# Optimization experiments

Measured on AMD Instinct MI355X. Metric: run time of the kernel, lower is better.

The kernel has to match this reference:

```python
import jax, jax.numpy as jnp
import numpy as np

B, N, D, V = 4096, 200, 128, 100000

def setup_inputs() -> dict:
    key = jax.random.key(0)
    k1, k2, k3, k4 = jax.random.split(key, 4)
    x = jax.random.normal(k1, (B, D), dtype=jnp.float32)
    candidates = jax.random.randint(k2, (B, N), 0, V, dtype=jnp.int64)
    W_mu = jax.random.normal(k3, (D, D), dtype=jnp.float32) * (1.0 / np.sqrt(D))
    b_mu = jnp.zeros((D,), dtype=jnp.float32)
    mu_bias = jnp.zeros((V,), dtype=jnp.float32)
    emb_table = jax.random.normal(k4, (V, D), dtype=jnp.float32) * 0.02
    return {"x": x, "candidates": candidates, "W_mu": W_mu, "b_mu": b_mu,
            "mu_bias": mu_bias, "emb_table": emb_table}

def reference(x, candidates, W_mu, b_mu, mu_bias, emb_table):
    # mu_head: Linear(d_model, d_model) followed by exact (erf) GELU
    h = jax.nn.gelu(x @ W_mu + b_mu, approximate=False)          # (B, D)
    emb = emb_table[candidates]                                  # (B, N, D) gather
    logits = jnp.einsum('bd,bnd->bn', h, emb)                    # batched dot product
    logits = logits + mu_bias[candidates]                        # bias gather-add
    return logits
```

## Files before the change

kernel.cpp:

```cpp
#include <hip/hip_runtime.h>
#include <hip/hip_bf16.h>
#include <math.h>


#define BDIM 4096
#define NCAND 200
#define DDIM 128

__global__ __launch_bounds__(256) void gelu_head_kernel(
    const float* __restrict__ x, const float* __restrict__ W,
    const float* __restrict__ bvec, float* __restrict__ h) {
  __shared__ float xs[8][DDIM];
  const int b0 = blockIdx.x * 8;
  const int t = threadIdx.x;

  {
    const float4* xg = reinterpret_cast<const float4*>(x + (size_t)b0 * DDIM);
    float4* xsv = reinterpret_cast<float4*>(&xs[0][0]);
    xsv[t] = xg[t];
  }
  __syncthreads();

  const int col = t & 127;
  const int rp = t >> 7;
  float acc0 = 0.f, acc1 = 0.f, acc2 = 0.f, acc3 = 0.f;
#pragma unroll 8
  for (int k = 0; k < DDIM; ++k) {
    const float w = W[k * DDIM + col];
    acc0 = fmaf(xs[rp + 0][k], w, acc0);
    acc1 = fmaf(xs[rp + 2][k], w, acc1);
    acc2 = fmaf(xs[rp + 4][k], w, acc2);
    acc3 = fmaf(xs[rp + 6][k], w, acc3);
  }
  const float bb = bvec[col];
  float v[4] = {acc0 + bb, acc1 + bb, acc2 + bb, acc3 + bb};
#pragma unroll
  for (int r = 0; r < 4; ++r) {
    const float u = v[r];
    const float g = 0.5f * u * (1.0f + erff(u * 0.70710678118654752f));
    h[(size_t)(b0 + rp + 2 * r) * DDIM + col] = g;
  }
}

__global__ __launch_bounds__(256) void gather_dot_kernel(
    const float* __restrict__ h, const int* __restrict__ cand,
    const float* __restrict__ bias, const float* __restrict__ emb,
    float* __restrict__ out) {
  const int wave = (blockIdx.x * 256 + threadIdx.x) >> 6;
  const int lane = threadIdx.x & 63;
  const int b = wave >> 1;
  const int half = wave & 1;
  const int l16 = lane & 15;
  const int grp = lane >> 4;

  const float4* hv = reinterpret_cast<const float4*>(h + (size_t)b * DDIM);
  const float4 h1 = hv[l16];
  const float4 h2 = hv[l16 + 16];

  const int nstart = half * 100;
  const int nend = nstart + 100;
  const int rowbase = b * NCAND;

  for (int n0 = nstart; n0 < nend; n0 += 64) {
    const int nseg = min(64, nend - n0);
    int ci = 0;
    float bi = 0.f;
    if (lane < nseg) {
      ci = cand[rowbase + n0 + lane];
      bi = bias[ci];
    }
    const int iters = nseg >> 2;
#pragma unroll 4
    for (int i = 0; i < iters; ++i) {
      const int slot = i * 4 + grp;
      const int c = __shfl(ci, slot);
      const float4* ev = reinterpret_cast<const float4*>(emb + (size_t)c * DDIM);
      const float4 v1 = ev[l16];
      const float4 v2 = ev[l16 + 16];
      float acc = v1.x * h1.x;
      acc = fmaf(v1.y, h1.y, acc);
      acc = fmaf(v1.z, h1.z, acc);
      acc = fmaf(v1.w, h1.w, acc);
      acc = fmaf(v2.x, h2.x, acc);
      acc = fmaf(v2.y, h2.y, acc);
      acc = fmaf(v2.z, h2.z, acc);
      acc = fmaf(v2.w, h2.w, acc);
      acc += __shfl_xor(acc, 1);
      acc += __shfl_xor(acc, 2);
      acc += __shfl_xor(acc, 4);
      acc += __shfl_xor(acc, 8);
      const float bslot = __shfl(bi, slot);
      if (l16 == 0) out[rowbase + n0 + slot] = acc + bslot;
    }
  }
}

extern "C" void kernel_launch(void* const* d_in, const int* in_sizes, int n_in,
                              void* d_out, int out_size, void* d_ws, size_t ws_size,
                              hipStream_t stream) {
  const float* x = (const float*)d_in[0];
  const int* candidates = (const int*)d_in[1];
  const float* W_mu = (const float*)d_in[2];
  const float* b_mu = (const float*)d_in[3];
  const float* mu_bias = (const float*)d_in[4];
  const float* emb_table = (const float*)d_in[5];
  float* out = (float*)d_out;

  float* h = (float*)d_ws;

  gelu_head_kernel<<<BDIM / 8, 256, 0, stream>>>(x, W_mu, b_mu, h);
  gather_dot_kernel<<<(BDIM * 2) / 4, 256, 0, stream>>>(h, candidates, mu_bias,
                                                        emb_table, out);
}
```

Baseline: 157.5 us.

## Invert candidate gather into per-vocab CSR grouping via histogram, scan, scatter

```diff
diff --git a/kernel.cpp b/kernel.cpp
--- a/kernel.cpp
+++ b/kernel.cpp
@@ -6,6 +6,11 @@
 #define BDIM 4096
 #define NCAND 200
 #define DDIM 128
+#define VOCAB 100000
+#define NPAIRS (BDIM * NCAND)
+#define NSB ((VOCAB + 1023) / 1024)
+
+typedef unsigned int u32;
 
 __global__ __launch_bounds__(256) void gelu_head_kernel(
     const float* __restrict__ x, const float* __restrict__ W,
@@ -13,14 +18,12 @@
   __shared__ float xs[8][DDIM];
   const int b0 = blockIdx.x * 8;
   const int t = threadIdx.x;
-
   {
     const float4* xg = reinterpret_cast<const float4*>(x + (size_t)b0 * DDIM);
     float4* xsv = reinterpret_cast<float4*>(&xs[0][0]);
     xsv[t] = xg[t];
   }
   __syncthreads();
-
   const int col = t & 127;
   const int rp = t >> 7;
   float acc0 = 0.f, acc1 = 0.f, acc2 = 0.f, acc3 = 0.f;
@@ -42,6 +45,121 @@
   }
 }
 
+__global__ __launch_bounds__(256) void hist_kernel(const int* __restrict__ cand,
+                                                   u32* __restrict__ counts) {
+  const int i = blockIdx.x * 256 + threadIdx.x;
+  if (i < NPAIRS) atomicAdd(&counts[cand[i]], 1u);
+}
+
+__global__ __launch_bounds__(256) void scan1_kernel(const u32* __restrict__ counts,
+                                                    u32* __restrict__ offsets,
+                                                    u32* __restrict__ partials) {
+  __shared__ u32 sh[256];
+  const int tid = threadIdx.x;
+  const int base = blockIdx.x * 1024 + tid * 4;
+  u32 v0 = (base + 0 < VOCAB) ? counts[base + 0] : 0u;
+  u32 v1 = (base + 1 < VOCAB) ? counts[base + 1] : 0u;
+  u32 v2 = (base + 2 < VOCAB) ? counts[base + 2] : 0u;
+  u32 v3 = (base + 3 < VOCAB) ? counts[base + 3] : 0u;
+  const u32 s = v0 + v1 + v2 + v3;
+  sh[tid] = s;
+  __syncthreads();
+  for (int off = 1; off < 256; off <<= 1) {
+    const u32 t = (tid >= off) ? sh[tid - off] : 0u;
+    __syncthreads();
+    sh[tid] += t;
+    __syncthreads();
+  }
+  u32 excl = sh[tid] - s;
+  if (tid == 255) partials[blockIdx.x] = sh[255];
+  if (base + 0 < VOCAB) offsets[base + 0] = excl;
+  excl += v0;
+  if (base + 1 < VOCAB) offsets[base + 1] = excl;
+  excl += v1;
+  if (base + 2 < VOCAB) offsets[base + 2] = excl;
+  excl += v2;
+  if (base + 3 < VOCAB) offsets[base + 3] = excl;
+}
+
+__global__ __launch_bounds__(256) void scan2_kernel(u32* __restrict__ partials) {
+  __shared__ u32 sh[256];
+  const int tid = threadIdx.x;
+  const u32 p = (tid < NSB) ? partials[tid] : 0u;
+  sh[tid] = p;
+  __syncthreads();
+  for (int off = 1; off < 256; off <<= 1) {
+    const u32 t = (tid >= off) ? sh[tid - off] : 0u;
+    __syncthreads();
+    sh[tid] += t;
+    __syncthreads();
+  }
+  if (tid < NSB) partials[tid] = sh[tid] - p;
+}
+
+__global__ __launch_bounds__(256) void scan_add_kernel(u32* __restrict__ offsets,
+                                                       const u32* __restrict__ partials,
+                                                       u32* __restrict__ cursors) {
+  const int i = blockIdx.x * 256 + threadIdx.x;
+  if (i < VOCAB) {
+    const u32 v = offsets[i] + partials[i >> 10];
+    offsets[i] = v;
+    cursors[i] = v;
+  }
+  if (i == VOCAB) offsets[VOCAB] = (u32)NPAIRS;
+}
+
+__global__ __launch_bounds__(256) void scatter_kernel(const int* __restrict__ cand,
+                                                      u32* __restrict__ cursors,
+                                                      u32* __restrict__ pairs) {
+  const int i = blockIdx.x * 256 + threadIdx.x;
+  if (i < NPAIRS) {
+    const u32 c = (u32)cand[i];
+    const u32 pos = atomicAdd(&cursors[c], 1u);
+    pairs[pos] = (u32)i;
+  }
+}
+
+__global__ __launch_bounds__(256) void vocab_dot_kernel(
+    const float* __restrict__ h, const float* __restrict__ emb,
+    const float* __restrict__ bias, const u32* __restrict__ offsets,
+    const u32* __restrict__ pairs, float* __restrict__ out) {
+  const int wid = (blockIdx.x * 256 + threadIdx.x) >> 6;
+  if (wid >= VOCAB) return;
+  const int lane = threadIdx.x & 63;
+  const int l16 = lane & 15;
+  const int grp = lane >> 4;
+
+  const float4* ev = reinterpret_cast<const float4*>(emb + (size_t)wid * DDIM);
+  const float4 e1 = ev[l16];
+  const float4 e2 = ev[l16 + 16];
+  const float bv = bias[wid];
+  const u32 start = offsets[wid];
+  const u32 end = offsets[wid + 1];
+
+  for (u32 j0 = start; j0 < end; j0 += 4) {
+    const u32 jj = j0 + (u32)grp;
+    const bool m = jj < end;
+    const u32 idx = pairs[m ? jj : (end - 1)];
+    const u32 b = idx / 200u;
+    const float4* hv = reinterpret_cast<const float4*>(h + (size_t)b * DDIM);
+    const float4 h1 = hv[l16];
+    const float4 h2 = hv[l16 + 16];
+    float acc = e1.x * h1.x;
+    acc = fmaf(e1.y, h1.y, acc);
+    acc = fmaf(e1.z, h1.z, acc);
+    acc = fmaf(e1.w, h1.w, acc);
+    acc = fmaf(e2.x, h2.x, acc);
+    acc = fmaf(e2.y, h2.y, acc);
+    acc = fmaf(e2.z, h2.z, acc);
+    acc = fmaf(e2.w, h2.w, acc);
+    acc += __shfl_xor(acc, 1);
+    acc += __shfl_xor(acc, 2);
+    acc += __shfl_xor(acc, 4);
+    acc += __shfl_xor(acc, 8);
+    if (l16 == 0 && m) out[idx] = acc + bv;
+  }
+}
+
 __global__ __launch_bounds__(256) void gather_dot_kernel(
     const float* __restrict__ h, const int* __restrict__ cand,
     const float* __restrict__ bias, const float* __restrict__ emb,
@@ -52,15 +170,12 @@
   const int half = wave & 1;
   const int l16 = lane & 15;
   const int grp = lane >> 4;
-
   const float4* hv = reinterpret_cast<const float4*>(h + (size_t)b * DDIM);
   const float4 h1 = hv[l16];
   const float4 h2 = hv[l16 + 16];
-
   const int nstart = half * 100;
   const int nend = nstart + 100;
   const int rowbase = b * NCAND;
-
   for (int n0 = nstart; n0 < nend; n0 += 64) {
     const int nseg = min(64, nend - n0);
     int ci = 0;
@@ -106,9 +221,33 @@
   const float* emb_table = (const float*)d_in[5];
   float* out = (float*)d_out;
 
-  float* h = (float*)d_ws;
+  char* ws = (char*)d_ws;
+  size_t off = 0;
+  float* h = (float*)(ws + off);
+  off += (size_t)BDIM * DDIM * 4;
+  u32* counts = (u32*)(ws + off);
+  off += ((VOCAB * 4 + 255) / 256) * 256;
+  u32* offsets = (u32*)(ws + off);
+  off += (((VOCAB + 1) * 4 + 255) / 256) * 256;
+  u32* partials = (u32*)(ws + off);
+  off += 4096;
+  u32* pairs = (u32*)(ws + off);
+  off += (size_t)NPAIRS * 4;
+  const size_t needed = off;
 
   gelu_head_kernel<<<BDIM / 8, 256, 0, stream>>>(x, W_mu, b_mu, h);
-  gather_dot_kernel<<<(BDIM * 2) / 4, 256, 0, stream>>>(h, candidates, mu_bias,
-                                                        emb_table, out);
-}
+
+  if (ws_size >= needed) {
+    hipMemsetAsync(counts, 0, (size_t)VOCAB * 4, stream);
+    hist_kernel<<<NPAIRS / 256, 256, 0, stream>>>(candidates, counts);
+    scan1_kernel<<<NSB, 256, 0, stream>>>(counts, offsets, partials);
+    scan2_kernel<<<1, 256, 0, stream>>>(partials);
+    scan_add_kernel<<<(VOCAB + 256) / 256, 256, 0, stream>>>(offsets, partials, counts);
+    scatter_kernel<<<NPAIRS / 256, 256, 0, stream>>>(candidates, counts, pairs);
+    vocab_dot_kernel<<<(VOCAB * 64) / 256, 256, 0, stream>>>(h, emb_table, mu_bias,
+                                                             offsets, pairs, out);
+  } else {
+    gather_dot_kernel<<<(BDIM * 2) / 4, 256, 0, stream>>>(h, candidates, mu_bias,
+                                                          emb_table, out);
+  }
+}
```

Measured after the change: 246.3 us. +56.4%, slower.

## Fuse GELU head and gather-dot into one kernel with h kept in LDS

Applied to the files above, without the earlier changes.

```diff
diff --git a/kernel.cpp b/kernel.cpp
--- a/kernel.cpp
+++ b/kernel.cpp
@@ -1,5 +1,4 @@
 #include <hip/hip_runtime.h>
-#include <hip/hip_bf16.h>
 #include <math.h>
 
 
@@ -7,55 +6,43 @@
 #define NCAND 200
 #define DDIM 128
 
-__global__ __launch_bounds__(256) void gelu_head_kernel(
-    const float* __restrict__ x, const float* __restrict__ W,
-    const float* __restrict__ bvec, float* __restrict__ h) {
-  __shared__ float xs[8][DDIM];
-  const int b0 = blockIdx.x * 8;
+__global__ __launch_bounds__(256) void fused_head_dot(
+    const float* __restrict__ x, const int* __restrict__ cand,
+    const float* __restrict__ W, const float* __restrict__ bvec,
+    const float* __restrict__ bias, const float* __restrict__ emb,
+    float* __restrict__ out) {
+  __shared__ float xs[2][DDIM];
+  __shared__ float hs[2][DDIM];
   const int t = threadIdx.x;
+  const int b0 = blockIdx.x * 2;
 
+  if (t < 64) {
+    reinterpret_cast<float4*>(&xs[0][0])[t] =
+        reinterpret_cast<const float4*>(x + (size_t)b0 * DDIM)[t];
+  }
+  __syncthreads();
   {
-    const float4* xg = reinterpret_cast<const float4*>(x + (size_t)b0 * DDIM);
-    float4* xsv = reinterpret_cast<float4*>(&xs[0][0]);
-    xsv[t] = xg[t];
+    const int col = t & 127;
+    const int rr = t >> 7;
+    float acc = 0.f;
+#pragma unroll 8
+    for (int k = 0; k < DDIM; ++k)
+      acc = fmaf(xs[rr][k], W[k * DDIM + col], acc);
+    acc += bvec[col];
+    hs[rr][col] = 0.5f * acc * (1.0f + erff(acc * 0.70710678118654752f));
   }
   __syncthreads();
 
-  const int col = t & 127;
-  const int rp = t >> 7;
-  float acc0 = 0.f, acc1 = 0.f, acc2 = 0.f, acc3 = 0.f;
-#pragma unroll 8
-  for (int k = 0; k < DDIM; ++k) {
-    const float w = W[k * DDIM + col];
-    acc0 = fmaf(xs[rp + 0][k], w, acc0);
-    acc1 = fmaf(xs[rp + 2][k], w, acc1);
-    acc2 = fmaf(xs[rp + 4][k], w, acc2);
-    acc3 = fmaf(xs[rp + 6][k], w, acc3);
-  }
-  const float bb = bvec[col];
-  float v[4] = {acc0 + bb, acc1 + bb, acc2 + bb, acc3 + bb};
-#pragma unroll
-  for (int r = 0; r < 4; ++r) {
-    const float u = v[r];
-    const float g = 0.5f * u * (1.0f + erff(u * 0.70710678118654752f));
-    h[(size_t)(b0 + rp + 2 * r) * DDIM + col] = g;
-  }
-}
-
-__global__ __launch_bounds__(256) void gather_dot_kernel(
-    const float* __restrict__ h, const int* __restrict__ cand,
-    const float* __restrict__ bias, const float* __restrict__ emb,
-    float* __restrict__ out) {
-  const int wave = (blockIdx.x * 256 + threadIdx.x) >> 6;
-  const int lane = threadIdx.x & 63;
-  const int b = wave >> 1;
-  const int half = wave & 1;
+  const int wv = t >> 6;
+  const int lane = t & 63;
   const int l16 = lane & 15;
   const int grp = lane >> 4;
+  const int r = wv >> 1;
+  const int half = wv & 1;
+  const int b = b0 + r;
 
-  const float4* hv = reinterpret_cast<const float4*>(h + (size_t)b * DDIM);
-  const float4 h1 = hv[l16];
-  const float4 h2 = hv[l16 + 16];
+  const float4 h1 = reinterpret_cast<const float4*>(&hs[r][0])[l16];
+  const float4 h2 = reinterpret_cast<const float4*>(&hs[r][0])[l16 + 16];
 
   const int nstart = half * 100;
   const int nend = nstart + 100;
@@ -64,10 +51,10 @@
   for (int n0 = nstart; n0 < nend; n0 += 64) {
     const int nseg = min(64, nend - n0);
     int ci = 0;
-    float bi = 0.f;
+    float bv = 0.f;
     if (lane < nseg) {
       ci = cand[rowbase + n0 + lane];
-      bi = bias[ci];
+      bv = bias[ci];
     }
     const int iters = nseg >> 2;
 #pragma unroll 4
@@ -89,7 +76,7 @@
       acc += __shfl_xor(acc, 2);
       acc += __shfl_xor(acc, 4);
       acc += __shfl_xor(acc, 8);
-      const float bslot = __shfl(bi, slot);
+      const float bslot = __shfl(bv, slot);
       if (l16 == 0) out[rowbase + n0 + slot] = acc + bslot;
     }
   }
@@ -106,9 +93,6 @@
   const float* emb_table = (const float*)d_in[5];
   float* out = (float*)d_out;
 
-  float* h = (float*)d_ws;
-
-  gelu_head_kernel<<<BDIM / 8, 256, 0, stream>>>(x, W_mu, b_mu, h);
-  gather_dot_kernel<<<(BDIM * 2) / 4, 256, 0, stream>>>(h, candidates, mu_bias,
-                                                        emb_table, out);
+  fused_head_dot<<<BDIM / 2, 256, 0, stream>>>(x, candidates, W_mu, b_mu,
+                                               mu_bias, emb_table, out);
 }
```

New measurement: 153.7 us. -2.4%, faster.
